# Kernel tuning notes

Measured on AMD Instinct MI355X. Metric: run time of the kernel, lower is better.

Reference implementation:

```python
import jax, jax.numpy as jnp
import numpy as np

CHEBYSHEV_K = 5  # number of Chebyshev polynomial terms


def setup_inputs() -> dict:
    key = jax.random.key(0)
    k1, k2, k3 = jax.random.split(key, 3)
    B, N, F_in, F_out = 1024, 512, 16, 8
    x = jax.random.normal(k1, (B, N, F_in), dtype=jnp.float32)
    # symmetric scaled-Laplacian-like matrix, scaled small so recurrence stays stable
    A = jax.random.normal(k2, (N, N), dtype=jnp.float32) / jnp.sqrt(jnp.float32(N))
    L = 0.5 * (A + A.T)
    # xavier-uniform-like weights [K, F_in, F_out]
    limit = np.sqrt(6.0 / (F_in + F_out)).astype(np.float32)
    W = jax.random.uniform(k3, (CHEBYSHEV_K, F_in, F_out), dtype=jnp.float32,
                           minval=-limit, maxval=limit)
    b = jnp.zeros((F_out,), dtype=jnp.float32)
    return {"x": x, "L": L, "W": W, "b": b}


def reference(x, L, W, b):
    # x: [B, N, F_in], L: [N, N], W: [K, F_in, F_out], b: [F_out]
    Lx = lambda z: jnp.einsum('nm,bmf->bnf', L, z)
    Z0 = x
    Z1 = Lx(x)
    out = Z0 @ W[0] + Z1 @ W[1]
    for k in range(2, CHEBYSHEV_K):  # small fixed K, structural loop
        Zk = 2.0 * Lx(Z1) - Z0
        out = out + Zk @ W[k]
        Z0, Z1 = Z1, Zk
    return out + b
```

## Files before the change

kernel.cpp:

```cpp
#include <hip/hip_runtime.h>
#include <cstdint>
#include <cstddef>


typedef __attribute__((ext_vector_type(8))) short  frag_ab;
typedef __attribute__((ext_vector_type(4))) float  frag_cd;

constexpr int BN  = 512;
constexpr int FIN = 16;
constexpr int FOUT= 8;
constexpr int GK  = 5 * BN;
constexpr int LDST= BN + 8;
constexpr int ZBUF= 64 * LDST;

__device__ __forceinline__ uint16_t f2bf(float f) {
    uint32_t u = __builtin_bit_cast(uint32_t, f);
    u += 0x7FFFu + ((u >> 16) & 1u);
    return (uint16_t)(u >> 16);
}
__device__ __forceinline__ float bf2f(uint16_t h) {
    uint32_t u = ((uint32_t)h) << 16;
    return __builtin_bit_cast(float, u);
}

__device__ __forceinline__ size_t pfrag(int mt, int g, int lane) {
    return ((size_t)(mt * 80 + g) * 64 + lane) * 8;
}
__device__ __forceinline__ size_t pelem(int k, int row, int col) {
    return pfrag(row >> 4, k * 16 + (col >> 5),
                 ((col >> 3) & 3) * 16 + (row & 15)) + (col & 7);
}
__device__ __forceinline__ size_t lfrag16(int mt, int kt, int lane) {
    return ((size_t)(mt * 16 + kt) * 64 + lane) * 8;
}
__device__ __forceinline__ size_t aswz(int row, int k) {
    return lfrag16(row >> 4, k >> 5, ((k >> 3) & 3) * 16 + (row & 15)) + (k & 7);
}


__global__ __launch_bounds__(256)
void cvtP(const float* __restrict__ Lf, uint16_t* __restrict__ Pcat,
          uint16_t* __restrict__ Llo) {
    int t = blockIdx.x * 256 + threadIdx.x;
    int lane = t & 63, f = t >> 6;
    int mt = f >> 4, kt = f & 15;
    int row = mt * 16 + (lane & 15);
    int k0  = kt * 32 + (lane >> 4) * 8;
    const float4* p = reinterpret_cast<const float4*>(Lf + (size_t)row * BN + k0);
    float4 u0 = p[0], u1 = p[1];
    float v[8] = {u0.x, u0.y, u0.z, u0.w, u1.x, u1.y, u1.z, u1.w};
    frag_ab hi, lo;
#pragma unroll
    for (int j = 0; j < 8; ++j) {
        uint16_t h = f2bf(v[j]);
        hi[j] = (short)h;
        lo[j] = (short)f2bf(v[j] - bf2f(h));
    }
    *reinterpret_cast<frag_ab*>(Pcat + pfrag(mt, 16 + kt, lane)) = hi;
    *reinterpret_cast<frag_ab*>(Llo + lfrag16(mt, kt, lane)) = lo;
}

__global__ __launch_bounds__(256)
void pfill(uint16_t* __restrict__ Pcat) {
    int t = blockIdx.x * 256 + threadIdx.x;
    int lane = t & 63, f = t >> 6;
    int mt = f >> 4, kt = f & 15;
    int row = mt * 16 + (lane & 15);
    int kb  = kt * 32 + (lane >> 4) * 8;
    frag_ab o;
#pragma unroll
    for (int j = 0; j < 8; ++j) o[j] = (short)((row == kb + j) ? 0x3F80 : 0);
    *reinterpret_cast<frag_ab*>(Pcat + pfrag(mt, kt, lane)) = o;
}

__global__ __launch_bounds__(256)
void pstep(uint16_t* __restrict__ Pcat, const uint16_t* __restrict__ Llo,
           int dstk, int srck, int subk) {
    int tid = threadIdx.x, wv = tid >> 6, lane = tid & 63;
    int lr = lane & 15, q = lane >> 4;
    int it = blockIdx.x * 4 + wv;
    int to = it >> 5, jt = it & 31;
    frag_cd acc = {0.f, 0.f, 0.f, 0.f};
    for (int ks = 0; ks < 16; ++ks) {
        frag_ab ah = *reinterpret_cast<const frag_ab*>(Pcat + pfrag(to, 16 + ks, lane));
        frag_ab al = *reinterpret_cast<const frag_ab*>(Llo + lfrag16(to, ks, lane));
        frag_ab b  = *reinterpret_cast<const frag_ab*>(Pcat + pfrag(jt, srck * 16 + ks, lane));
        acc = __builtin_amdgcn_mfma_f32_16x16x32_bf16(ah, b, acc, 0, 0, 0);
        acc = __builtin_amdgcn_mfma_f32_16x16x32_bf16(al, b, acc, 0, 0, 0);
    }
#pragma unroll
    for (int r = 0; r < 4; ++r) {
        int row = to * 16 + q * 4 + r, col = jt * 16 + lr;
        float s = (subk < 0) ? ((row == col) ? 1.f : 0.f)
                             : bf2f(Pcat[pelem(subk, row, col)]);
        Pcat[pelem(dstk, row, col)] = f2bf(2.f * acc[r] - s);
    }
}

__global__ __launch_bounds__(256)
void ycat(const float* __restrict__ x, const float* __restrict__ W,
          uint16_t* __restrict__ Y) {
    int tid = threadIdx.x;
    int bb = tid >> 7, l = tid & 127;
    int b = blockIdx.x * 2 + bb;
    const float* xb = x + (size_t)b * (BN * FIN);
    float xf[4][16];
#pragma unroll
    for (int mm = 0; mm < 4; ++mm)
#pragma unroll
        for (int fi = 0; fi < 4; ++fi) {
            float4 u = *reinterpret_cast<const float4*>(xb + (size_t)(mm * 128 + l) * 16 + fi * 4);
            xf[mm][fi * 4 + 0] = u.x; xf[mm][fi * 4 + 1] = u.y;
            xf[mm][fi * 4 + 2] = u.z; xf[mm][fi * 4 + 3] = u.w;
        }
    uint16_t* yb = Y + (size_t)b * 8 * GK;
#pragma unroll
    for (int k = 0; k < 5; ++k) {
#pragma unroll
        for (int fo = 0; fo < 8; ++fo) {
            float a0 = 0.f, a1 = 0.f, a2 = 0.f, a3 = 0.f;
#pragma unroll
            for (int f = 0; f < 16; ++f) {
                float w = W[(k * 16 + f) * 8 + fo];
                a0 += xf[0][f] * w; a1 += xf[1][f] * w;
                a2 += xf[2][f] * w; a3 += xf[3][f] * w;
            }
            uint16_t* yr = yb + (size_t)fo * GK + k * 512 + l;
            yr[0]   = f2bf(a0); yr[128] = f2bf(a1);
            yr[256] = f2bf(a2); yr[384] = f2bf(a3);
        }
    }
}

__global__ __launch_bounds__(512, 2)
void chebgemm(const uint16_t* __restrict__ Pcat, const uint16_t* __restrict__ Y,
              const float* __restrict__ bvec, float* __restrict__ out) {
    __shared__ uint16_t lds[34816];
    uint16_t* a0 = lds;
    uint16_t* a1 = lds + 8192;
    uint16_t* b0 = lds + 16384;
    uint16_t* b1 = lds + 25600;

    int bid = blockIdx.x;
    int wg  = (bid & 7) * 32 + (bid >> 3);
    int mtB = wg >> 6;
    int jtB = wg & 63;
    int m0  = mtB * 128;
    int j0  = jtB * 128;

    int tid = threadIdx.x, wv = tid >> 6, lane = tid & 63;
    int lr = lane & 15, q = lane >> 4;
    int wm = wv >> 2, wj = wv & 3;

    frag_cd acc[4][2] = {};
    frag_ab rA[2], rB[2];

    auto loadA = [&](int c) {
#pragma unroll
        for (int s = 0; s < 2; ++s) {
            int idx = tid + s * 512;
            int piece = idx >> 6, ln = idx & 63;
            int amt = piece >> 1, kk = piece & 1;
            rA[s] = *reinterpret_cast<const frag_ab*>(
                Pcat + pfrag(mtB * 8 + amt, c * 2 + kk, ln));
        }
    };
    auto loadB = [&](int c) {
#pragma unroll
        for (int s = 0; s < 2; ++s) {
            int idx = tid + s * 512;
            int jj = idx >> 3, c8 = idx & 7;
            rB[s] = *reinterpret_cast<const frag_ab*>(
                Y + (size_t)(j0 + jj) * GK + c * 64 + c8 * 8);
        }
    };
    auto writeS = [&](uint16_t* ab, uint16_t* bb) {
#pragma unroll
        for (int s = 0; s < 2; ++s) {
            int idx = tid + s * 512;
            *reinterpret_cast<frag_ab*>(ab + (size_t)idx * 8) = rA[s];
            int jj = idx >> 3, c8 = idx & 7;
            *reinterpret_cast<frag_ab*>(bb + (size_t)jj * 72 + c8 * 8) = rB[s];
        }
    };
    auto compute = [&](const uint16_t* ab, const uint16_t* bb) {
#pragma unroll
        for (int ksub = 0; ksub < 2; ++ksub) {
            frag_ab aF[4], bF[2];
#pragma unroll
            for (int mi = 0; mi < 4; ++mi)
                aF[mi] = *reinterpret_cast<const frag_ab*>(
                    ab + (size_t)(((wm * 4 + mi) * 2 + ksub) * 64 + lane) * 8);
#pragma unroll
            for (int cj = 0; cj < 2; ++cj)
                bF[cj] = *reinterpret_cast<const frag_ab*>(
                    bb + (size_t)(wj * 32 + cj * 16 + lr) * 72 + ksub * 32 + q * 8);
#pragma unroll
            for (int mi = 0; mi < 4; ++mi)
#pragma unroll
                for (int cj = 0; cj < 2; ++cj)
                    acc[mi][cj] = __builtin_amdgcn_mfma_f32_16x16x32_bf16(
                        aF[mi], bF[cj], acc[mi][cj], 0, 0, 0);
        }
    };

    loadA(0); loadB(0);
    writeS(a0, b0);
    __syncthreads();
    for (int c = 0; c < 40; ++c) {
        bool odd = (c & 1) != 0;
        const uint16_t* ap = odd ? a1 : a0;
        const uint16_t* bp = odd ? b1 : b0;
        uint16_t* an = odd ? a0 : a1;
        uint16_t* bn = odd ? b0 : b1;
        if (c < 39) { loadA(c + 1); loadB(c + 1); }
        compute(ap, bp);
        if (c < 39) writeS(an, bn);
        __syncthreads();
    }

    float* fbuf = reinterpret_cast<float*>(lds);
#pragma unroll
    for (int mi = 0; mi < 4; ++mi)
#pragma unroll
        for (int cj = 0; cj < 2; ++cj) {
            int jl = wj * 32 + cj * 16 + lr;
#pragma unroll
            for (int r = 0; r < 4; ++r) {
                int nl = wm * 64 + mi * 16 + q * 4 + r;
                fbuf[nl * 128 + jl] = acc[mi][cj][r];
            }
        }
    __syncthreads();
    float4 bv0 = *reinterpret_cast<const float4*>(bvec);
    float4 bv1 = *(reinterpret_cast<const float4*>(bvec) + 1);
#pragma unroll
    for (int i = 0; i < 8; ++i) {
        int L = i * 2048 + tid * 4;
        int bb = L >> 10, r = L & 1023, nn = r >> 3, fo = r & 7;
        float4 v = *reinterpret_cast<const float4*>(fbuf + nn * 128 + bb * 8 + fo);
        float4 bias = (fo & 4) ? bv1 : bv0;
        v.x += bias.x; v.y += bias.y; v.z += bias.z; v.w += bias.w;
        *reinterpret_cast<float4*>(out + (size_t)(j0 / 8 + bb) * 4096
                                       + (size_t)(m0 + nn) * 8 + fo) = v;
    }
}


__global__ __launch_bounds__(256)
void cvtL_swz(const float* __restrict__ Lf, uint16_t* __restrict__ Lb) {
    int t = blockIdx.x * 256 + threadIdx.x;
    int f = t >> 6, lane = t & 63;
    int mt = f >> 4, ks = f & 15;
    int row = mt * 16 + (lane & 15);
    int k0  = ks * 32 + (lane >> 4) * 8;
    const float4* p = reinterpret_cast<const float4*>(Lf + (size_t)row * BN + k0);
    float4 u0 = p[0], u1 = p[1];
    frag_ab o;
    o[0] = (short)f2bf(u0.x); o[1] = (short)f2bf(u0.y);
    o[2] = (short)f2bf(u0.z); o[3] = (short)f2bf(u0.w);
    o[4] = (short)f2bf(u1.x); o[5] = (short)f2bf(u1.y);
    o[6] = (short)f2bf(u1.z); o[7] = (short)f2bf(u1.w);
    *reinterpret_cast<frag_ab*>(Lb + (size_t)t * 8) = o;
}

__global__ __launch_bounds__(256)
void m2comp(const float* __restrict__ Lf, uint16_t* __restrict__ Mb) {
    const int tid = threadIdx.x;
    const int wv = tid >> 6, lane = tid & 63, lr = lane & 15, q = lane >> 4;
    const int i0 = (blockIdx.x >> 4) * 32 + (wv >> 1) * 16;
    const int j0 = (blockIdx.x & 15) * 32 + (wv & 1) * 16;
    frag_cd acc = {0.f, 0.f, 0.f, 0.f};
    const float* arow = Lf + (size_t)(i0 + lr) * BN;
    const float* brow = Lf + (size_t)(j0 + lr) * BN;
    for (int ks = 0; ks < 16; ++ks) {
        const int kb = ks * 32 + q * 8;
        const float4* ap = reinterpret_cast<const float4*>(arow + kb);
        const float4* bp = reinterpret_cast<const float4*>(brow + kb);
        float4 A0 = ap[0], A1 = ap[1], B0 = bp[0], B1 = bp[1];
        float av[8]  = {A0.x, A0.y, A0.z, A0.w, A1.x, A1.y, A1.z, A1.w};
        float bw[8]  = {B0.x, B0.y, B0.z, B0.w, B1.x, B1.y, B1.z, B1.w};
        frag_ab ah, al, bh, bl;
#pragma unroll
        for (int j = 0; j < 8; ++j) {
            uint16_t h = f2bf(av[j]);
            ah[j] = (short)h; al[j] = (short)f2bf(av[j] - bf2f(h));
            uint16_t g = f2bf(bw[j]);
            bh[j] = (short)g; bl[j] = (short)f2bf(bw[j] - bf2f(g));
        }
        acc = __builtin_amdgcn_mfma_f32_16x16x32_bf16(ah, bh, acc, 0, 0, 0);
        acc = __builtin_amdgcn_mfma_f32_16x16x32_bf16(ah, bl, acc, 0, 0, 0);
        acc = __builtin_amdgcn_mfma_f32_16x16x32_bf16(al, bh, acc, 0, 0, 0);
    }
#pragma unroll
    for (int r = 0; r < 4; ++r) {
        int i = i0 + q * 4 + r, j = j0 + lr;
        float v = 2.f * acc[r] - ((i == j) ? 1.f : 0.f);
        Mb[aswz(i, j)] = f2bf(v);
    }
}

__global__ __launch_bounds__(512, 2)
void cheb2_kernel(const float* __restrict__ x, const uint16_t* __restrict__ Lb,
                  const uint16_t* __restrict__ Mb, const float* __restrict__ W,
                  const float* __restrict__ bvec, float* __restrict__ out) {
    __shared__ uint16_t ldsb[2 * ZBUF];
    uint16_t* z0 = ldsb;
    uint16_t* z1 = ldsb + ZBUF;
    const int tid = threadIdx.x, wave = tid >> 6, lane = tid & 63;
    const int lr = lane & 15, q = lane >> 4;

    const float4* x4 = reinterpret_cast<const float4*>(x + (size_t)blockIdx.x * (4 * BN * FIN));
    for (int s = 0; s < 2; ++s) {
        int a = tid + s * 512;
        int f0g = a & 3, n8 = (a >> 2) & 63, bl = a >> 8;
        int jb = bl * 2048 + n8 * 32 + f0g;
        float4 v[8];
#pragma unroll
        for (int r = 0; r < 8; ++r) v[r] = x4[jb + r * 4];
        int cb = bl * 16 + f0g * 4, nb = n8 * 8;
#pragma unroll
        for (int w = 0; w < 4; ++w) {
            frag_ab pk;
#pragma unroll
            for (int r = 0; r < 8; ++r)
                pk[r] = (short)f2bf(reinterpret_cast<const float*>(&v[r])[w]);
            *reinterpret_cast<frag_ab*>(&z0[(cb + w) * LDST + nb]) = pk;
        }
    }
    frag_ab wf[3];
#pragma unroll
    for (int p = 0; p < 3; ++p) {
        frag_ab t;
#pragma unroll
        for (int jj = 0; jj < 8; ++jj) {
            int k = q * 8 + jj, ki = p * 2 + (k >> 4), fin = k & 15;
            float val = 0.0f;
            if (lr < 8) {
                int idx = fin * FOUT + lr;
                if      (ki == 0) val = W[idx] - W[4 * 128 + idx];
                else if (ki == 1) val = W[128 + idx] - W[3 * 128 + idx];
                else if (ki < 5)  val = W[ki * 128 + idx];
            }
            t[jj] = (short)f2bf(val);
        }
        wf[p] = t;
    }
    const float bv = (lr < 8) ? bvec[lr] : 0.0f;
    frag_cd accOut[4][4] = {};
    frag_cd acc1[4][4], acc2[4][4];

    auto round = [&](const uint16_t* cur) {
#pragma unroll
        for (int mi = 0; mi < 4; ++mi)
#pragma unroll
            for (int ct = 0; ct < 4; ++ct) {
                acc1[mi][ct] = (frag_cd){0.f, 0.f, 0.f, 0.f};
                acc2[mi][ct] = (frag_cd){0.f, 0.f, 0.f, 0.f};
            }
        for (int ks = 0; ks < 16; ++ks) {
            frag_ab bfr[4];
#pragma unroll
            for (int ct = 0; ct < 4; ++ct)
                bfr[ct] = *reinterpret_cast<const frag_ab*>(
                    cur + (ct * 16 + lr) * LDST + ks * 32 + q * 8);
#pragma unroll
            for (int mi = 0; mi < 4; ++mi) {
                frag_ab a = *reinterpret_cast<const frag_ab*>(
                    Lb + lfrag16(wave + mi * 8, ks, lane));
                frag_ab m = *reinterpret_cast<const frag_ab*>(
                    Mb + lfrag16(wave + mi * 8, ks, lane));
#pragma unroll
                for (int ct = 0; ct < 4; ++ct)
                    acc1[mi][ct] = __builtin_amdgcn_mfma_f32_16x16x32_bf16(
                        a, bfr[ct], acc1[mi][ct], 0, 0, 0);
#pragma unroll
                for (int ct = 0; ct < 4; ++ct)
                    acc2[mi][ct] = __builtin_amdgcn_mfma_f32_16x16x32_bf16(
                        m, bfr[ct], acc2[mi][ct], 0, 0, 0);
            }
        }
    };
    auto wb = [&](frag_cd (&acc)[4][4], uint16_t* dst, float scale) {
#pragma unroll
        for (int mi = 0; mi < 4; ++mi) {
            int row0 = (wave + mi * 8) * 16 + q * 4;
#pragma unroll
            for (int ct = 0; ct < 4; ++ct) {
                uint16_t* dp = dst + (ct * 16 + lr) * LDST + row0;
                ushort4 nv;
                nv.x = f2bf(scale * acc[mi][ct][0]); nv.y = f2bf(scale * acc[mi][ct][1]);
                nv.z = f2bf(scale * acc[mi][ct][2]); nv.w = f2bf(scale * acc[mi][ct][3]);
                *reinterpret_cast<ushort4*>(dp) = nv;
            }
        }
    };
    auto epi = [&](const uint16_t* bA, const uint16_t* bB, frag_ab wfr) {
        const uint16_t* base = (q < 2) ? bA : bB;
        int finb = (q & 1) * 8;
#pragma unroll
        for (int mi = 0; mi < 4; ++mi) {
            int n = (wave + mi * 8) * 16 + lr;
#pragma unroll
            for (int bt = 0; bt < 4; ++bt) {
                const uint16_t* pp = base + (bt * 16 + finb) * LDST + n;
                frag_ab afr;
#pragma unroll
                for (int jj = 0; jj < 8; ++jj) afr[jj] = (short)pp[jj * LDST];
                accOut[mi][bt] = __builtin_amdgcn_mfma_f32_16x16x32_bf16(
                    afr, wfr, accOut[mi][bt], 0, 0, 0);
            }
        }
    };

    __syncthreads();
    round(z0);
    wb(acc1, z1, 1.f);
    __syncthreads();
    epi(z0, z1, wf[0]);
    __syncthreads();
    wb(acc2, z0, 1.f);
    __syncthreads();
    round(z0);
    wb(acc1, z1, 2.f);
    __syncthreads();
    epi(z0, z1, wf[1]);
    __syncthreads();
    wb(acc2, z0, 2.f);
    __syncthreads();
    epi(z0, z0, wf[2]);

    float* fbuf = reinterpret_cast<float*>(z1);
    if (lr < 8) {
#pragma unroll
        for (int mi = 0; mi < 4; ++mi) {
            int n0 = (wave + mi * 8) * 16 + q * 4;
#pragma unroll
            for (int bt = 0; bt < 4; ++bt)
#pragma unroll
                for (int r = 0; r < 4; ++r)
                    fbuf[(bt * BN + n0 + r) * FOUT + lr] = accOut[mi][bt][r] + bv;
        }
    }
    __syncthreads();
    {
        const float4* fb4 = reinterpret_cast<const float4*>(fbuf);
        float4* o4 = reinterpret_cast<float4*>(out + (size_t)blockIdx.x * (4 * BN * FOUT));
#pragma unroll
        for (int i = 0; i < 8; ++i)
            o4[i * 512 + tid] = fb4[i * 512 + tid];
    }
}

__global__ __launch_bounds__(512, 2)
void cheb1_kernel(const float* __restrict__ x, const float* __restrict__ Lf,
                  const float* __restrict__ W, const float* __restrict__ bvec,
                  float* __restrict__ out) {
    __shared__ uint16_t ldsb[2 * ZBUF];
    uint16_t* z0 = ldsb;
    uint16_t* z1 = ldsb + ZBUF;
    const int tid = threadIdx.x, wave = tid >> 6, lane = tid & 63;
    const int lr = lane & 15, q = lane >> 4;
    const float4* x4 = reinterpret_cast<const float4*>(x + (size_t)blockIdx.x * (4 * BN * FIN));
    for (int s = 0; s < 2; ++s) {
        int a = tid + s * 512;
        int f0g = a & 3, n8 = (a >> 2) & 63, bl = a >> 8;
        int jb = bl * 2048 + n8 * 32 + f0g;
        float4 v[8];
#pragma unroll
        for (int r = 0; r < 8; ++r) v[r] = x4[jb + r * 4];
        int cb = bl * 16 + f0g * 4, nb = n8 * 8;
#pragma unroll
        for (int w = 0; w < 4; ++w) {
            frag_ab pk;
#pragma unroll
            for (int r = 0; r < 8; ++r)
                pk[r] = (short)f2bf(reinterpret_cast<const float*>(&v[r])[w]);
            *reinterpret_cast<frag_ab*>(&z0[(cb + w) * LDST + nb]) = pk;
        }
    }
    frag_ab wf[3];
#pragma unroll
    for (int p = 0; p < 3; ++p) {
        frag_ab t;
#pragma unroll
        for (int jj = 0; jj < 8; ++jj) {
            int k = q * 8 + jj, ki = p * 2 + (k >> 4), fin = k & 15;
            float val = (lr < 8 && ki < 5) ? W[ki * 128 + fin * FOUT + lr] : 0.0f;
            t[jj] = (short)f2bf(val);
        }
        wf[p] = t;
    }
    const float bv = (lr < 8) ? bvec[lr] : 0.0f;
    frag_cd accOut[4][4] = {};
    auto loadA = [&](int mt, int ks) -> frag_ab {
        const float4* p = reinterpret_cast<const float4*>(Lf + (size_t)(mt * 16 + lr) * BN + ks * 32 + q * 8);
        float4 u0 = p[0], u1 = p[1];
        frag_ab t;
        t[0] = (short)f2bf(u0.x); t[1] = (short)f2bf(u0.y);
        t[2] = (short)f2bf(u0.z); t[3] = (short)f2bf(u0.w);
        t[4] = (short)f2bf(u1.x); t[5] = (short)f2bf(u1.y);
        t[6] = (short)f2bf(u1.z); t[7] = (short)f2bf(u1.w);
        return t;
    };
    auto app = [&](const uint16_t* cur, uint16_t* dst, bool first) {
        frag_cd acc[4][4] = {};
        for (int ks = 0; ks < 16; ++ks) {
            frag_ab bfr[4];
#pragma unroll
            for (int ct = 0; ct < 4; ++ct)
                bfr[ct] = *reinterpret_cast<const frag_ab*>(
                    cur + (ct * 16 + lr) * LDST + ks * 32 + q * 8);
#pragma unroll
            for (int mi = 0; mi < 4; ++mi) {
                frag_ab a = loadA(wave + mi * 8, ks);
#pragma unroll
                for (int ct = 0; ct < 4; ++ct)
                    acc[mi][ct] = __builtin_amdgcn_mfma_f32_16x16x32_bf16(
                        a, bfr[ct], acc[mi][ct], 0, 0, 0);
            }
        }
#pragma unroll
        for (int mi = 0; mi < 4; ++mi) {
            int row0 = (wave + mi * 8) * 16 + q * 4;
#pragma unroll
            for (int ct = 0; ct < 4; ++ct) {
                uint16_t* dp = dst + (ct * 16 + lr) * LDST + row0;
                float pz[4] = {0.f, 0.f, 0.f, 0.f};
                if (!first) {
                    ushort4 pv = *reinterpret_cast<const ushort4*>(dp);
                    pz[0] = bf2f(pv.x); pz[1] = bf2f(pv.y);
                    pz[2] = bf2f(pv.z); pz[3] = bf2f(pv.w);
                }
                ushort4 nv;
                float v0 = acc[mi][ct][0], v1 = acc[mi][ct][1];
                float v2 = acc[mi][ct][2], v3 = acc[mi][ct][3];
                if (!first) { v0 = 2.f*v0-pz[0]; v1 = 2.f*v1-pz[1];
                              v2 = 2.f*v2-pz[2]; v3 = 2.f*v3-pz[3]; }
                nv.x = f2bf(v0); nv.y = f2bf(v1); nv.z = f2bf(v2); nv.w = f2bf(v3);
                *reinterpret_cast<ushort4*>(dp) = nv;
            }
        }
    };
    auto epi = [&](const uint16_t* bA, const uint16_t* bB, frag_ab wfr) {
        const uint16_t* base = (q < 2) ? bA : bB;
        int finb = (q & 1) * 8;
#pragma unroll
        for (int mi = 0; mi < 4; ++mi) {
            int n = (wave + mi * 8) * 16 + lr;
#pragma unroll
            for (int bt = 0; bt < 4; ++bt) {
                const uint16_t* pp = base + (bt * 16 + finb) * LDST + n;
                frag_ab afr;
#pragma unroll
                for (int jj = 0; jj < 8; ++jj) afr[jj] = (short)pp[jj * LDST];
                accOut[mi][bt] = __builtin_amdgcn_mfma_f32_16x16x32_bf16(
                    afr, wfr, accOut[mi][bt], 0, 0, 0);
            }
        }
    };
    __syncthreads();
    app(z0, z1, true);  __syncthreads();
    epi(z0, z1, wf[0]); __syncthreads();
    app(z1, z0, false); __syncthreads();
    app(z0, z1, false); __syncthreads();
    epi(z0, z1, wf[1]); __syncthreads();
    app(z1, z0, false); __syncthreads();
    epi(z0, z0, wf[2]);
    if (lr < 8) {
        float* ob = out + (size_t)blockIdx.x * 4 * BN * FOUT;
#pragma unroll
        for (int mi = 0; mi < 4; ++mi) {
            int row0 = (wave + mi * 8) * 16 + q * 4;
#pragma unroll
            for (int bt = 0; bt < 4; ++bt) {
                float* op = ob + bt * (BN * FOUT) + row0 * FOUT + lr;
                op[0] = accOut[mi][bt][0] + bv; op[FOUT] = accOut[mi][bt][1] + bv;
                op[2 * FOUT] = accOut[mi][bt][2] + bv; op[3 * FOUT] = accOut[mi][bt][3] + bv;
            }
        }
    }
}

extern "C" void kernel_launch(void* const* d_in, const int* in_sizes, int n_in,
                              void* d_out, int out_size, void* d_ws, size_t ws_size,
                              hipStream_t stream) {
    const float* x  = (const float*)d_in[0];
    const float* Lf = (const float*)d_in[1];
    const float* W  = (const float*)d_in[2];
    const float* bv = (const float*)d_in[3];
    float* out = (float*)d_out;

    const size_t PCAT_B = (size_t)32 * 80 * 64 * 8 * 2;
    const size_t LLO_B  = (size_t)BN * BN * 2;
    const size_t YC_B   = (size_t)8192 * GK * 2;
    const size_t matB   = (size_t)BN * BN * 2;

    if (ws_size >= PCAT_B + LLO_B + YC_B) {
        uint16_t* Pcat = (uint16_t*)d_ws;
        uint16_t* Llo  = Pcat + PCAT_B / 2;
        uint16_t* Yc   = Pcat + (PCAT_B + LLO_B) / 2;
        cvtP  <<<dim3(128), dim3(256), 0, stream>>>(Lf, Pcat, Llo);
        pfill <<<dim3(128), dim3(256), 0, stream>>>(Pcat);
        pstep <<<dim3(256), dim3(256), 0, stream>>>(Pcat, Llo, 2, 1, -1);
        pstep <<<dim3(256), dim3(256), 0, stream>>>(Pcat, Llo, 3, 2, 1);
        pstep <<<dim3(256), dim3(256), 0, stream>>>(Pcat, Llo, 4, 3, 2);
        ycat  <<<dim3(512), dim3(256), 0, stream>>>(x, W, Yc);
        chebgemm<<<dim3(256), dim3(512), 0, stream>>>(Pcat, Yc, bv, out);
    } else if (ws_size >= 2 * matB) {
        uint16_t* Lb = (uint16_t*)d_ws;
        uint16_t* Mb = Lb + (size_t)BN * BN;
        cvtL_swz<<<dim3(128), dim3(256), 0, stream>>>(Lf, Lb);
        m2comp  <<<dim3(256), dim3(256), 0, stream>>>(Lf, Mb);
        cheb2_kernel<<<dim3(256), dim3(512), 0, stream>>>(x, Lb, Mb, W, bv, out);
    } else {
        cheb1_kernel<<<dim3(256), dim3(512), 0, stream>>>(x, Lf, W, bv, out);
    }
}
```

Before: 163.0 us.

## Compute P3,P4 from P2 in parallel, drop identity term, fuse prep kernels

Precomputes the Chebyshev polynomials with a shorter chain: P2 is computed once with split hi/lo precision, then P3 = 2·L·P2 − L and P4 = 2·P2·P2 − I are computed together in one launch instead of two sequential steps. The P0 = I block is dropped from the GEMM and replaced by adding the Y0 term in the epilogue, which shrinks the K dimension from 2560 to 2048. The x·W projection and the L conversion are fused into a single prep launch, and Y is written in MFMA fragment layout so chebgemm reads its fragments directly from global memory with no LDS double buffering. This removes kernel launches and serial dependencies, at the cost of relying on cache for fragment reuse, which may hurt load latency hiding in the main GEMM.

Result: faster. 150.9 us (-7.4%).

```diff
diff --git a/kernel.cpp b/kernel.cpp
--- a/kernel.cpp
+++ b/kernel.cpp
@@ -10,6 +10,7 @@
 constexpr int FIN = 16;
 constexpr int FOUT= 8;
 constexpr int GK  = 5 * BN;
+constexpr int PG  = 64;
 constexpr int LDST= BN + 8;
 constexpr int ZBUF= 64 * LDST;
 
@@ -24,10 +25,10 @@
 }
 
 __device__ __forceinline__ size_t pfrag(int mt, int g, int lane) {
-    return ((size_t)(mt * 80 + g) * 64 + lane) * 8;
+    return ((size_t)(mt * PG + g) * 64 + lane) * 8;
 }
 __device__ __forceinline__ size_t pelem(int k, int row, int col) {
-    return pfrag(row >> 4, k * 16 + (col >> 5),
+    return pfrag(row >> 4, (k - 1) * 16 + (col >> 5),
                  ((col >> 3) & 3) * 16 + (row & 15)) + (col & 7);
 }
 __device__ __forceinline__ size_t lfrag16(int mt, int kt, int lane) {
@@ -36,199 +37,183 @@
 __device__ __forceinline__ size_t aswz(int row, int k) {
     return lfrag16(row >> 4, k >> 5, ((k >> 3) & 3) * 16 + (row & 15)) + (k & 7);
 }
-
+__device__ __forceinline__ size_t yfrag(int jt16, int g, int lane) {
+    return ((size_t)(jt16 * 80 + g) * 64 + lane) * 8;
+}
 
 __global__ __launch_bounds__(256)
-void cvtP(const float* __restrict__ Lf, uint16_t* __restrict__ Pcat,
-          uint16_t* __restrict__ Llo) {
-    int t = blockIdx.x * 256 + threadIdx.x;
-    int lane = t & 63, f = t >> 6;
-    int mt = f >> 4, kt = f & 15;
-    int row = mt * 16 + (lane & 15);
-    int k0  = kt * 32 + (lane >> 4) * 8;
-    const float4* p = reinterpret_cast<const float4*>(Lf + (size_t)row * BN + k0);
-    float4 u0 = p[0], u1 = p[1];
-    float v[8] = {u0.x, u0.y, u0.z, u0.w, u1.x, u1.y, u1.z, u1.w};
-    frag_ab hi, lo;
-#pragma unroll
-    for (int j = 0; j < 8; ++j) {
-        uint16_t h = f2bf(v[j]);
-        hi[j] = (short)h;
-        lo[j] = (short)f2bf(v[j] - bf2f(h));
-    }
-    *reinterpret_cast<frag_ab*>(Pcat + pfrag(mt, 16 + kt, lane)) = hi;
-    *reinterpret_cast<frag_ab*>(Llo + lfrag16(mt, kt, lane)) = lo;
-}
-
-__global__ __launch_bounds__(256)
-void pfill(uint16_t* __restrict__ Pcat) {
-    int t = blockIdx.x * 256 + threadIdx.x;
-    int lane = t & 63, f = t >> 6;
-    int mt = f >> 4, kt = f & 15;
-    int row = mt * 16 + (lane & 15);
-    int kb  = kt * 32 + (lane >> 4) * 8;
-    frag_ab o;
-#pragma unroll
-    for (int j = 0; j < 8; ++j) o[j] = (short)((row == kb + j) ? 0x3F80 : 0);
-    *reinterpret_cast<frag_ab*>(Pcat + pfrag(mt, kt, lane)) = o;
-}
-
-__global__ __launch_bounds__(256)
-void pstep(uint16_t* __restrict__ Pcat, const uint16_t* __restrict__ Llo,
-           int dstk, int srck, int subk) {
+void prep(const float* __restrict__ x, const float* __restrict__ Lf,
+          const float* __restrict__ W, uint16_t* __restrict__ Pcat,
+          uint16_t* __restrict__ Llo, uint16_t* __restrict__ Yf) {
+    int bid = blockIdx.x, tid = threadIdx.x;
+    if (bid < 2048) {
+        int t = bid * 256 + tid;
+        int jlow = t & 15;
+        int moct = (t >> 4) & 63;
+        int jhi  = t >> 10;
+        int b  = jhi * 2 + (jlow >> 3);
+        int fo = jlow & 7;
+        int m0 = moct * 8;
+        float wr[5][16];
+#pragma unroll
+        for (int k = 0; k < 5; ++k)
+#pragma unroll
+            for (int f = 0; f < 16; ++f)
+                wr[k][f] = W[(k * 16 + f) * 8 + fo];
+        float tmp[5][8];
+        const float* xb = x + (size_t)b * (BN * FIN) + (size_t)m0 * FIN;
+#pragma unroll
+        for (int r = 0; r < 8; ++r) {
+            float xr[16];
+#pragma unroll
+            for (int fi = 0; fi < 4; ++fi) {
+                float4 u = *reinterpret_cast<const float4*>(xb + r * FIN + fi * 4);
+                xr[fi * 4 + 0] = u.x; xr[fi * 4 + 1] = u.y;
+                xr[fi * 4 + 2] = u.z; xr[fi * 4 + 3] = u.w;
+            }
+#pragma unroll
+            for (int k = 0; k < 5; ++k) {
+                float s = 0.f;
+#pragma unroll
+                for (int f = 0; f < 16; ++f) s += xr[f] * wr[k][f];
+                tmp[k][r] = s;
+            }
+        }
+#pragma unroll
+        for (int k = 0; k < 5; ++k) {
+            frag_ab o;
+#pragma unroll
+            for (int j = 0; j < 8; ++j) o[j] = (short)f2bf(tmp[k][j]);
+            *reinterpret_cast<frag_ab*>(
+                Yf + yfrag(jhi, k * 16 + (moct >> 2), (moct & 3) * 16 + jlow)) = o;
+        }
+    } else {
+        int t = (bid - 2048) * 256 + tid;
+        int lane = t & 63, f = t >> 6;
+        int mt = f >> 4, kt = f & 15;
+        int row = mt * 16 + (lane & 15);
+        int k0  = kt * 32 + (lane >> 4) * 8;
+        const float4* p = reinterpret_cast<const float4*>(Lf + (size_t)row * BN + k0);
+        float4 u0 = p[0], u1 = p[1];
+        float v[8] = {u0.x, u0.y, u0.z, u0.w, u1.x, u1.y, u1.z, u1.w};
+        frag_ab hi, lo;
+#pragma unroll
+        for (int j = 0; j < 8; ++j) {
+            uint16_t h = f2bf(v[j]);
+            hi[j] = (short)h;
+            lo[j] = (short)f2bf(v[j] - bf2f(h));
+        }
+        *reinterpret_cast<frag_ab*>(Pcat + pfrag(mt, kt, lane)) = hi;
+        *reinterpret_cast<frag_ab*>(Llo + lfrag16(mt, kt, lane)) = lo;
+    }
+}
+
+__global__ __launch_bounds__(512)
+void p2k(uint16_t* __restrict__ Pcat, const uint16_t* __restrict__ Llo,
+         uint16_t* __restrict__ P2lo) {
     int tid = threadIdx.x, wv = tid >> 6, lane = tid & 63;
     int lr = lane & 15, q = lane >> 4;
-    int it = blockIdx.x * 4 + wv;
-    int to = it >> 5, jt = it & 31;
+    int id = blockIdx.x * 8 + wv;
+    int to = id >> 5, jt = id & 31;
     frag_cd acc = {0.f, 0.f, 0.f, 0.f};
+#pragma unroll
     for (int ks = 0; ks < 16; ++ks) {
-        frag_ab ah = *reinterpret_cast<const frag_ab*>(Pcat + pfrag(to, 16 + ks, lane));
-        frag_ab al = *reinterpret_cast<const frag_ab*>(Llo + lfrag16(to, ks, lane));
-        frag_ab b  = *reinterpret_cast<const frag_ab*>(Pcat + pfrag(jt, srck * 16 + ks, lane));
-        acc = __builtin_amdgcn_mfma_f32_16x16x32_bf16(ah, b, acc, 0, 0, 0);
-        acc = __builtin_amdgcn_mfma_f32_16x16x32_bf16(al, b, acc, 0, 0, 0);
+        frag_ab ahi = *reinterpret_cast<const frag_ab*>(Pcat + pfrag(to, ks, lane));
+        frag_ab alo = *reinterpret_cast<const frag_ab*>(Llo + lfrag16(to, ks, lane));
+        frag_ab bhi = *reinterpret_cast<const frag_ab*>(Pcat + pfrag(jt, ks, lane));
+        frag_ab blo = *reinterpret_cast<const frag_ab*>(Llo + lfrag16(jt, ks, lane));
+        acc = __builtin_amdgcn_mfma_f32_16x16x32_bf16(ahi, bhi, acc, 0, 0, 0);
+        acc = __builtin_amdgcn_mfma_f32_16x16x32_bf16(alo, bhi, acc, 0, 0, 0);
+        acc = __builtin_amdgcn_mfma_f32_16x16x32_bf16(ahi, blo, acc, 0, 0, 0);
     }
 #pragma unroll
     for (int r = 0; r < 4; ++r) {
         int row = to * 16 + q * 4 + r, col = jt * 16 + lr;
-        float s = (subk < 0) ? ((row == col) ? 1.f : 0.f)
-                             : bf2f(Pcat[pelem(subk, row, col)]);
-        Pcat[pelem(dstk, row, col)] = f2bf(2.f * acc[r] - s);
-    }
-}
-
-__global__ __launch_bounds__(256)
-void ycat(const float* __restrict__ x, const float* __restrict__ W,
-          uint16_t* __restrict__ Y) {
-    int tid = threadIdx.x;
-    int bb = tid >> 7, l = tid & 127;
-    int b = blockIdx.x * 2 + bb;
-    const float* xb = x + (size_t)b * (BN * FIN);
-    float xf[4][16];
-#pragma unroll
-    for (int mm = 0; mm < 4; ++mm)
-#pragma unroll
-        for (int fi = 0; fi < 4; ++fi) {
-            float4 u = *reinterpret_cast<const float4*>(xb + (size_t)(mm * 128 + l) * 16 + fi * 4);
-            xf[mm][fi * 4 + 0] = u.x; xf[mm][fi * 4 + 1] = u.y;
-            xf[mm][fi * 4 + 2] = u.z; xf[mm][fi * 4 + 3] = u.w;
-        }
-    uint16_t* yb = Y + (size_t)b * 8 * GK;
-#pragma unroll
-    for (int k = 0; k < 5; ++k) {
-#pragma unroll
-        for (int fo = 0; fo < 8; ++fo) {
-            float a0 = 0.f, a1 = 0.f, a2 = 0.f, a3 = 0.f;
-#pragma unroll
-            for (int f = 0; f < 16; ++f) {
-                float w = W[(k * 16 + f) * 8 + fo];
-                a0 += xf[0][f] * w; a1 += xf[1][f] * w;
-                a2 += xf[2][f] * w; a3 += xf[3][f] * w;
-            }
-            uint16_t* yr = yb + (size_t)fo * GK + k * 512 + l;
-            yr[0]   = f2bf(a0); yr[128] = f2bf(a1);
-            yr[256] = f2bf(a2); yr[384] = f2bf(a3);
-        }
-    }
-}
-
-__global__ __launch_bounds__(512, 2)
-void chebgemm(const uint16_t* __restrict__ Pcat, const uint16_t* __restrict__ Y,
+        float v = 2.f * acc[r] - ((row == col) ? 1.f : 0.f);
+        uint16_t h = f2bf(v);
+        Pcat[pelem(2, row, col)] = h;
+        P2lo[aswz(row, col)] = f2bf(v - bf2f(h));
+    }
+}
+
+__global__ __launch_bounds__(512)
+void p34k(uint16_t* __restrict__ Pcat, const uint16_t* __restrict__ Llo,
+          const uint16_t* __restrict__ P2lo) {
+    int tid = threadIdx.x, wv = tid >> 6, lane = tid & 63;
+    int lr = lane & 15, q = lane >> 4;
+    int id = blockIdx.x * 8 + wv;
+    bool isP3 = id < 1024;
+    int id2 = isP3 ? id : id - 1024;
+    int to = id2 >> 5, jt = id2 & 31;
+    int agoff = isP3 ? 0 : 16;
+    const uint16_t* aLo = isP3 ? Llo : P2lo;
+    frag_cd acc = {0.f, 0.f, 0.f, 0.f};
+#pragma unroll
+    for (int ks = 0; ks < 16; ++ks) {
+        frag_ab ahi = *reinterpret_cast<const frag_ab*>(Pcat + pfrag(to, agoff + ks, lane));
+        frag_ab alo = *reinterpret_cast<const frag_ab*>(aLo + lfrag16(to, ks, lane));
+        frag_ab bhi = *reinterpret_cast<const frag_ab*>(Pcat + pfrag(jt, 16 + ks, lane));
+        frag_ab blo = *reinterpret_cast<const frag_ab*>(P2lo + lfrag16(jt, ks, lane));
+        acc = __builtin_amdgcn_mfma_f32_16x16x32_bf16(ahi, bhi, acc, 0, 0, 0);
+        acc = __builtin_amdgcn_mfma_f32_16x16x32_bf16(alo, bhi, acc, 0, 0, 0);
+        acc = __builtin_amdgcn_mfma_f32_16x16x32_bf16(ahi, blo, acc, 0, 0, 0);
+    }
+#pragma unroll
+    for (int r = 0; r < 4; ++r) {
+        int row = to * 16 + q * 4 + r, col = jt * 16 + lr;
+        if (isP3) {
+            float sub = bf2f(Pcat[pelem(1, row, col)]) + bf2f(Llo[aswz(row, col)]);
+            Pcat[pelem(3, row, col)] = f2bf(2.f * acc[r] - sub);
+        } else {
+            float sub = (row == col) ? 1.f : 0.f;
+            Pcat[pelem(4, row, col)] = f2bf(2.f * acc[r] - sub);
+        }
+    }
+}
+
+__global__ __launch_bounds__(512)
+void chebgemm(const uint16_t* __restrict__ Pcat, const uint16_t* __restrict__ Yf,
               const float* __restrict__ bvec, float* __restrict__ out) {
-    __shared__ uint16_t lds[34816];
-    uint16_t* a0 = lds;
-    uint16_t* a1 = lds + 8192;
-    uint16_t* b0 = lds + 16384;
-    uint16_t* b1 = lds + 25600;
-
+    __shared__ float fbuf[16384];
     int bid = blockIdx.x;
-    int wg  = (bid & 7) * 32 + (bid >> 3);
-    int mtB = wg >> 6;
-    int jtB = wg & 63;
-    int m0  = mtB * 128;
-    int j0  = jtB * 128;
-
+    int xcd = bid & 7, n = bid >> 3;
+    int jt  = xcd * 8 + (n >> 2);
+    int mtB = n & 3;
     int tid = threadIdx.x, wv = tid >> 6, lane = tid & 63;
     int lr = lane & 15, q = lane >> 4;
     int wm = wv >> 2, wj = wv & 3;
 
     frag_cd acc[4][2] = {};
-    frag_ab rA[2], rB[2];
-
-    auto loadA = [&](int c) {
-#pragma unroll
-        for (int s = 0; s < 2; ++s) {
-            int idx = tid + s * 512;
-            int piece = idx >> 6, ln = idx & 63;
-            int amt = piece >> 1, kk = piece & 1;
-            rA[s] = *reinterpret_cast<const frag_ab*>(
-                Pcat + pfrag(mtB * 8 + amt, c * 2 + kk, ln));
-        }
-    };
-    auto loadB = [&](int c) {
-#pragma unroll
-        for (int s = 0; s < 2; ++s) {
-            int idx = tid + s * 512;
-            int jj = idx >> 3, c8 = idx & 7;
-            rB[s] = *reinterpret_cast<const frag_ab*>(
-                Y + (size_t)(j0 + jj) * GK + c * 64 + c8 * 8);
-        }
-    };
-    auto writeS = [&](uint16_t* ab, uint16_t* bb) {
-#pragma unroll
-        for (int s = 0; s < 2; ++s) {
-            int idx = tid + s * 512;
-            *reinterpret_cast<frag_ab*>(ab + (size_t)idx * 8) = rA[s];
-            int jj = idx >> 3, c8 = idx & 7;
-            *reinterpret_cast<frag_ab*>(bb + (size_t)jj * 72 + c8 * 8) = rB[s];
-        }
-    };
-    auto compute = [&](const uint16_t* ab, const uint16_t* bb) {
-#pragma unroll
-        for (int ksub = 0; ksub < 2; ++ksub) {
-            frag_ab aF[4], bF[2];
-#pragma unroll
-            for (int mi = 0; mi < 4; ++mi)
-                aF[mi] = *reinterpret_cast<const frag_ab*>(
-                    ab + (size_t)(((wm * 4 + mi) * 2 + ksub) * 64 + lane) * 8);
+#pragma unroll 2
+    for (int kt = 0; kt < 64; ++kt) {
+        frag_ab aF[4], bF[2];
+#pragma unroll
+        for (int mi = 0; mi < 4; ++mi)
+            aF[mi] = *reinterpret_cast<const frag_ab*>(
+                Pcat + pfrag(mtB * 8 + wm * 4 + mi, kt, lane));
+#pragma unroll
+        for (int cj = 0; cj < 2; ++cj)
+            bF[cj] = *reinterpret_cast<const frag_ab*>(
+                Yf + yfrag(jt * 8 + wj * 2 + cj, 16 + kt, lane));
+#pragma unroll
+        for (int mi = 0; mi < 4; ++mi)
 #pragma unroll
             for (int cj = 0; cj < 2; ++cj)
-                bF[cj] = *reinterpret_cast<const frag_ab*>(
-                    bb + (size_t)(wj * 32 + cj * 16 + lr) * 72 + ksub * 32 + q * 8);
-#pragma unroll
-            for (int mi = 0; mi < 4; ++mi)
-#pragma unroll
-                for (int cj = 0; cj < 2; ++cj)
-                    acc[mi][cj] = __builtin_amdgcn_mfma_f32_16x16x32_bf16(
-                        aF[mi], bF[cj], acc[mi][cj], 0, 0, 0);
-        }
-    };
-
-    loadA(0); loadB(0);
-    writeS(a0, b0);
-    __syncthreads();
-    for (int c = 0; c < 40; ++c) {
-        bool odd = (c & 1) != 0;
-        const uint16_t* ap = odd ? a1 : a0;
-        const uint16_t* bp = odd ? b1 : b0;
-        uint16_t* an = odd ? a0 : a1;
-        uint16_t* bn = odd ? b0 : b1;
-        if (c < 39) { loadA(c + 1); loadB(c + 1); }
-        compute(ap, bp);
-        if (c < 39) writeS(an, bn);
-        __syncthreads();
-    }
-
-    float* fbuf = reinterpret_cast<float*>(lds);
+                acc[mi][cj] = __builtin_amdgcn_mfma_f32_16x16x32_bf16(
+                    aF[mi], bF[cj], acc[mi][cj], 0, 0, 0);
+    }
 #pragma unroll
     for (int mi = 0; mi < 4; ++mi)
 #pragma unroll
         for (int cj = 0; cj < 2; ++cj) {
-            int jl = wj * 32 + cj * 16 + lr;
+            int jt16 = jt * 8 + wj * 2 + cj;
 #pragma unroll
             for (int r = 0; r < 4; ++r) {
-                int nl = wm * 64 + mi * 16 + q * 4 + r;
-                fbuf[nl * 128 + jl] = acc[mi][cj][r];
+                int nloc = wm * 64 + mi * 16 + q * 4 + r;
+                int ng = mtB * 128 + nloc;
+                float y0 = bf2f(Yf[yfrag(jt16, ng >> 5, ((ng >> 3) & 3) * 16 + lr)
+                                   + (ng & 7)]);
+                fbuf[nloc * 128 + wj * 32 + cj * 16 + lr] = acc[mi][cj][r] + y0;
             }
         }
     __syncthreads();
@@ -236,13 +221,13 @@
     float4 bv1 = *(reinterpret_cast<const float4*>(bvec) + 1);
 #pragma unroll
     for (int i = 0; i < 8; ++i) {
-        int L = i * 2048 + tid * 4;
-        int bb = L >> 10, r = L & 1023, nn = r >> 3, fo = r & 7;
+        int idx = i * 2048 + tid * 4;
+        int bb = idx >> 10, r = idx & 1023, nn = r >> 3, fo = r & 7;
         float4 v = *reinterpret_cast<const float4*>(fbuf + nn * 128 + bb * 8 + fo);
         float4 bias = (fo & 4) ? bv1 : bv0;
         v.x += bias.x; v.y += bias.y; v.z += bias.z; v.w += bias.w;
-        *reinterpret_cast<float4*>(out + (size_t)(j0 / 8 + bb) * 4096
-                                       + (size_t)(m0 + nn) * 8 + fo) = v;
+        *reinterpret_cast<float4*>(out + (size_t)(jt * 16 + bb) * 4096
+                                       + (size_t)(mtB * 128 + nn) * 8 + fo) = v;
     }
 }
 
@@ -278,8 +263,8 @@
         const float4* ap = reinterpret_cast<const float4*>(arow + kb);
         const float4* bp = reinterpret_cast<const float4*>(brow + kb);
         float4 A0 = ap[0], A1 = ap[1], B0 = bp[0], B1 = bp[1];
-        float av[8]  = {A0.x, A0.y, A0.z, A0.w, A1.x, A1.y, A1.z, A1.w};
-        float bw[8]  = {B0.x, B0.y, B0.z, B0.w, B1.x, B1.y, B1.z, B1.w};
+        float av[8] = {A0.x, A0.y, A0.z, A0.w, A1.x, A1.y, A1.z, A1.w};
+        float bw[8] = {B0.x, B0.y, B0.z, B0.w, B1.x, B1.y, B1.z, B1.w};
         frag_ab ah, al, bh, bl;
 #pragma unroll
         for (int j = 0; j < 8; ++j) {
@@ -591,22 +576,21 @@
     const float* bv = (const float*)d_in[3];
     float* out = (float*)d_out;
 
-    const size_t PCAT_B = (size_t)32 * 80 * 64 * 8 * 2;
+    const size_t PCAT_B = (size_t)32 * PG * 64 * 8 * 2;
     const size_t LLO_B  = (size_t)BN * BN * 2;
-    const size_t YC_B   = (size_t)8192 * GK * 2;
+    const size_t P2LO_B = LLO_B;
+    const size_t YF_B   = (size_t)512 * 80 * 64 * 8 * 2;
     const size_t matB   = (size_t)BN * BN * 2;
 
-    if (ws_size >= PCAT_B + LLO_B + YC_B) {
+    if (ws_size >= PCAT_B + LLO_B + P2LO_B + YF_B) {
         uint16_t* Pcat = (uint16_t*)d_ws;
         uint16_t* Llo  = Pcat + PCAT_B / 2;
-        uint16_t* Yc   = Pcat + (PCAT_B + LLO_B) / 2;
-        cvtP  <<<dim3(128), dim3(256), 0, stream>>>(Lf, Pcat, Llo);
-        pfill <<<dim3(128), dim3(256), 0, stream>>>(Pcat);
-        pstep <<<dim3(256), dim3(256), 0, stream>>>(Pcat, Llo, 2, 1, -1);
-        pstep <<<dim3(256), dim3(256), 0, stream>>>(Pcat, Llo, 3, 2, 1);
-        pstep <<<dim3(256), dim3(256), 0, stream>>>(Pcat, Llo, 4, 3, 2);
-        ycat  <<<dim3(512), dim3(256), 0, stream>>>(x, W, Yc);
-        chebgemm<<<dim3(256), dim3(512), 0, stream>>>(Pcat, Yc, bv, out);
+        uint16_t* P2lo = Pcat + (PCAT_B + LLO_B) / 2;
+        uint16_t* Yf   = Pcat + (PCAT_B + LLO_B + P2LO_B) / 2;
+        prep    <<<dim3(2176), dim3(256), 0, stream>>>(x, Lf, W, Pcat, Llo, Yf);
+        p2k     <<<dim3(128),  dim3(512), 0, stream>>>(Pcat, Llo, P2lo);
+        p34k    <<<dim3(256),  dim3(512), 0, stream>>>(Pcat, Llo, P2lo);
+        chebgemm<<<dim3(256),  dim3(512), 0, stream>>>(Pcat, Yf, bv, out);
     } else if (ws_size >= 2 * matB) {
         uint16_t* Lb = (uint16_t*)d_ws;
         uint16_t* Mb = Lb + (size_t)BN * BN;
```
